# Kernel optimization log

Hardware: AMD Instinct MI355X
Metric: run time of the kernel (lower is better)

The kernel has to match this reference:

```python
import jax, jax.numpy as jnp
import numpy as np

# ---------- constants ----------
EPS = 1e-5
_rng = np.random.default_rng(0)
_P = _rng.normal(size=(8, 3))
_P /= np.linalg.norm(_P, axis=1, keepdims=True)

def _y2_np(p):
    x, y, z = p[:, 0], p[:, 1], p[:, 2]
    return np.stack([x * y, y * z, 3 * z * z - 1, x * z, x * x - y * y], axis=-1)

_A2 = np.linalg.pinv(_y2_np(_P)).astype(np.float32)  # [5,8]
P_C = jnp.asarray(_P.astype(np.float32))
A2_C = jnp.asarray(_A2)
NORM_CONST = np.float32(1.0 / np.sqrt(20.0))  # avg_num_neighbors ** -0.5
# res update (buffer zeros, not learnable): sigmoid(0)=0.5
_U = 0.5
C_OLD = np.float32(1.0 / np.sqrt(_U * _U + 1.0))
C_NEW = np.float32(_U * C_OLD)


def _y2(p):  # real l=2 monomial basis on unit vectors
    x, y, z = p[..., 0], p[..., 1], p[..., 2]
    return jnp.stack([x * y, y * z, 3.0 * z * z - 1.0, x * z, x * x - y * y], axis=-1)


def _frame(v):  # [E,3] -> R [E,3,3] with R @ v_hat = z
    n = v / jnp.linalg.norm(v, axis=-1, keepdims=True)
    z = jnp.array([0.0, 0.0, 1.0], v.dtype)
    xa = jnp.array([1.0, 0.0, 0.0], v.dtype)
    a = jnp.where(jnp.abs(n[:, 2:3]) < 0.99, z, xa)
    e1 = jnp.cross(a, n)
    e1 = e1 / jnp.linalg.norm(e1, axis=-1, keepdims=True)
    e2 = jnp.cross(n, e1)
    return jnp.stack([e1, e2, n], axis=1)


def _wigner_d2(R):  # [E,3,3] -> D2 [E,5,5] via sample-point fit
    pts = jnp.einsum('pj,eij->epi', P_C, R)  # R @ p_k, [E,8,3]
    M = _y2(pts)  # [E,8,5] = Y_P @ D^T
    Dt = jnp.einsum('ap,epb->eab', A2_C, M)  # [E,5,5]
    return jnp.swapaxes(Dt, 1, 2)


def _sln(x, w0, b0, w1, w2):  # separable equivariant layernorm, 32x0e+16x1e+8x2e
    s = x[:, :32]
    v1 = x[:, 32:80].reshape(-1, 16, 3)
    v2 = x[:, 80:120].reshape(-1, 8, 5)
    mu = jnp.mean(s, axis=-1, keepdims=True)
    var = jnp.mean((s - mu) ** 2, axis=-1, keepdims=True)
    s = (s - mu) * jax.lax.rsqrt(var + EPS) * w0 + b0
    var1 = jnp.mean(v1 ** 2, axis=(1, 2))  # degree-balanced component variance
    var2 = jnp.mean(v2 ** 2, axis=(1, 2))
    inv = jax.lax.rsqrt(0.5 * (var1 + var2) + EPS)[:, None, None]
    v1 = v1 * inv * w1[None, :, None]
    v2 = v2 * inv * w2[None, :, None]
    return jnp.concatenate([s, v1.reshape(-1, 48), v2.reshape(-1, 40)], axis=-1)


def _ir_linear(x, W0, b0, W1, W2):  # irreps-wise linear 32x0e+16x1e+8x2e -> same
    s = x[:, :32] @ (W0 / np.sqrt(32.0)) + b0
    v1 = jnp.einsum('eui,uv->evi', x[:, 32:80].reshape(-1, 16, 3), W1) / np.sqrt(16.0)
    v2 = jnp.einsum('eui,uv->evi', x[:, 80:120].reshape(-1, 8, 5), W2) / np.sqrt(8.0)
    return jnp.concatenate([s, v1.reshape(-1, 48), v2.reshape(-1, 40)], axis=-1)


def _so2(x_cat, R, D2f, D2b, w):  # SO2 linear with per-edge dynamic weights
    E = x_cat.shape[0]
    w0 = w[:, :8960].reshape(E, 112, 80)
    w1r = w[:, 8960:10112].reshape(E, 48, 24)
    w1i = w[:, 10112:11264].reshape(E, 48, 24)
    w2r = w[:, 11264:11392].reshape(E, 16, 8)
    w2i = w[:, 11392:11520].reshape(E, 16, 8)
    # split concatenated [in + hidden] blocks
    s = jnp.concatenate([x_cat[:, :32], x_cat[:, 120:152]], axis=-1)  # [E,64]
    v1 = jnp.concatenate([x_cat[:, 32:80].reshape(E, 16, 3),
                          x_cat[:, 152:200].reshape(E, 16, 3)], axis=1)  # [E,32,3]
    v2 = jnp.concatenate([x_cat[:, 80:120].reshape(E, 8, 5),
                          x_cat[:, 200:240].reshape(E, 16 // 2, 5)], axis=1)  # [E,16,5]
    # rotate into edge-aligned frame
    v1 = jnp.einsum('eij,euj->eui', R, v1)
    v2 = jnp.einsum('eij,euj->eui', D2f, v2)
    in0 = jnp.concatenate([s, v1[:, :, 1], v2[:, :, 2]], axis=-1)   # m=0, [E,112]
    inn1 = jnp.concatenate([v1[:, :, 0], v2[:, :, 1]], axis=-1)     # m=-1, [E,48]
    inp1 = jnp.concatenate([v1[:, :, 2], v2[:, :, 3]], axis=-1)     # m=+1
    inn2 = v2[:, :, 0]  # m=-2
    inp2 = v2[:, :, 4]  # m=+2
    out0 = jnp.einsum('ei,eio->eo', in0, w0) / np.sqrt(112.0)
    op1 = (jnp.einsum('ei,eio->eo', inp1, w1r) - jnp.einsum('ei,eio->eo', inn1, w1i)) / np.sqrt(48.0)
    on1 = (jnp.einsum('ei,eio->eo', inn1, w1r) + jnp.einsum('ei,eio->eo', inp1, w1i)) / np.sqrt(48.0)
    op2 = (jnp.einsum('ei,eio->eo', inp2, w2r) - jnp.einsum('ei,eio->eo', inn2, w2i)) / np.sqrt(16.0)
    on2 = (jnp.einsum('ei,eio->eo', inn2, w2r) + jnp.einsum('ei,eio->eo', inp2, w2i)) / np.sqrt(16.0)
    s_out = out0[:, :56]
    y1 = jnp.stack([on1[:, :16], out0[:, 56:72], op1[:, :16]], axis=-1)  # [E,16,3]
    y2o = jnp.stack([on2, on1[:, 16:24], out0[:, 72:80], op1[:, 16:24], op2], axis=-1)  # [E,8,5]
    # rotate back
    y1 = jnp.einsum('eij,euj->eui', jnp.swapaxes(R, 1, 2), y1)
    y2o = jnp.einsum('eij,euj->eui', D2b, y2o)
    return jnp.concatenate([s_out, y1.reshape(E, 48), y2o.reshape(E, 40)], axis=-1)  # [E,144]


def _gate(m):  # 32x0e scalars | 24x0e gates | 16x1e+8x2e gated
    s = jax.nn.silu(m[:, :32])
    g = jax.nn.sigmoid(m[:, 32:56])
    v1 = m[:, 56:104].reshape(-1, 16, 3) * g[:, :16, None]
    v2 = m[:, 104:144].reshape(-1, 8, 5) * g[:, 16:24, None]
    return jnp.concatenate([s, v1.reshape(-1, 48), v2.reshape(-1, 40)], axis=-1)


def _env(m, we):  # E3ElementLinear: per-mul elementwise weights
    s = m[:, :32] * we[:, :32]
    v1 = m[:, 32:80].reshape(-1, 16, 3) * we[:, 32:48, None]
    v2 = m[:, 80:120].reshape(-1, 8, 5) * we[:, 48:56, None]
    return jnp.concatenate([s, v1.reshape(-1, 48), v2.reshape(-1, 40)], axis=-1)


def setup_inputs() -> dict:
    key = jax.random.key(0)
    ks = jax.random.split(key, 16)
    N, E, L = 512, 10240, 128
    inp = {
        'latents': jax.random.normal(ks[0], (E, L), jnp.float32),
        'node_features': jax.random.normal(ks[1], (N, 120), jnp.float32),
        'hidden_features': jax.random.normal(ks[2], (E, 120), jnp.float32),
        'node_onehot': jnp.ones((N, 16), jnp.float32),
        'edge_vector': jax.random.normal(ks[3], (E, 3), jnp.float32),
        'W_tp': jax.random.normal(ks[4], (L, 11520), jnp.float32),
        'W_env': jax.random.normal(ks[5], (L, 56), jnp.float32),
        'sln_w0': jnp.ones((32,), jnp.float32),
        'sln_b0': jnp.zeros((32,), jnp.float32),
        'sln_w1': jnp.ones((16,), jnp.float32),
        'sln_w2': jnp.ones((8,), jnp.float32),
        'Wp0': jax.random.normal(ks[6], (32, 32), jnp.float32),
        'bp0': jnp.zeros((32,), jnp.float32),
        'Wp1': jax.random.normal(ks[7], (16, 16), jnp.float32),
        'Wp2': jax.random.normal(ks[8], (8, 8), jnp.float32),
        'Wr0': jax.random.normal(ks[9], (32, 32), jnp.float32),
        'br0': jnp.zeros((32,), jnp.float32),
        'Wr1': jax.random.normal(ks[10], (16, 16), jnp.float32),
        'Wr2': jax.random.normal(ks[11], (8, 8), jnp.float32),
        'atom_type': jax.random.randint(ks[12], (N,), 0, 10, jnp.int32),
        'edge_index': jax.random.randint(ks[13], (2, E), 0, N, jnp.int32),
        'active_edges': jnp.arange(E, dtype=jnp.int32),
    }
    return inp


def reference(latents, node_features, hidden_features, node_onehot, edge_vector,
              W_tp, W_env, sln_w0, sln_b0, sln_w1, sln_w2,
              Wp0, bp0, Wp1, Wp2, Wr0, br0, Wr1, Wr2,
              atom_type, edge_index, active_edges):
    n_nodes = node_features.shape[0]
    center = edge_index[0][active_edges]
    nf = _sln(node_features, sln_w0, sln_b0, sln_w1, sln_w2)
    x_cat = jnp.concatenate([nf[center], hidden_features], axis=-1)  # [E,240]
    v = edge_vector[active_edges]
    R = _frame(v)
    D2f = _wigner_d2(R)
    D2b = _wigner_d2(jnp.swapaxes(R, 1, 2))
    wdyn = latents @ (W_tp / np.sqrt(128.0))  # per-edge dynamic SO2 weights
    msg = _so2(x_cat, R, D2f, D2b, wdyn)
    msg = _gate(msg)
    msg = _ir_linear(msg, Wp0, bp0, Wp1, Wp2)
    wenv = latents[active_edges] @ (W_env / np.sqrt(128.0))
    weighted = _env(msg, wenv)
    new_nf = jax.ops.segment_sum(weighted, center, num_segments=n_nodes)
    new_nf = new_nf * NORM_CONST
    res = _ir_linear(node_features, Wr0, br0, Wr1, Wr2)
    return C_NEW * new_nf + C_OLD * res
```

## Files before the change

### kernel.cpp

```cpp
#include <hip/hip_runtime.h>
#include <math.h>

#define E_TOT   10240
#define N_NODES 512
#define NCOL    11520

typedef unsigned short ushort_t;
typedef unsigned int   uint_t;
typedef __bf16 bf16x8 __attribute__((ext_vector_type(8)));
typedef float  f32x4  __attribute__((ext_vector_type(4)));

constexpr float EPSF        = 1e-5f;
constexpr float INV_SQRT128 = 0.08838834764831845f;
constexpr float INV_SQRT112 = 0.09449111825230681f;
constexpr float INV_SQRT48  = 0.14433756729740643f;
constexpr float INV_SQRT32  = 0.17677669529663687f;
constexpr float INV_SQRT16  = 0.25f;
constexpr float INV_SQRT8   = 0.35355339059327373f;
constexpr float SC0 = INV_SQRT128 * INV_SQRT112;
constexpr float SC1 = INV_SQRT128 * INV_SQRT48;
constexpr float SC2 = INV_SQRT128 * INV_SQRT16;
constexpr float C_OLD_ = 0.8944271909999159f;
constexpr float C_NEW_ = 0.4472135954999579f;
constexpr float NORMC  = 0.22360679774997896f;

__device__ __forceinline__ float wsum(float v) {
#pragma unroll
  for (int off = 32; off > 0; off >>= 1) v += __shfl_xor(v, off, 64);
  return v;
}

__device__ __forceinline__ ushort_t f2bf(float x) {
  uint_t u = __float_as_uint(x);
  u = (u + 0x7fffu + ((u >> 16) & 1u)) >> 16;
  return (ushort_t)u;
}

__device__ __forceinline__ void wigner5(const float q[9], float D[25]) {
  const float q0x=q[0],q0y=q[1],q0z=q[2];
  const float q1x=q[3],q1y=q[4],q1z=q[5];
  const float q2x=q[6],q2y=q[7],q2z=q[8];
  D[0]  = q0x*q1y + q1x*q0y;
  D[1]  = q0y*q1z + q1y*q0z;
  D[2]  = 0.5f*(q0z*q1z);
  D[3]  = q0x*q1z + q1x*q0z;
  D[4]  = 0.5f*(q0x*q1x - q0y*q1y);
  D[5]  = q1x*q2y + q2x*q1y;
  D[6]  = q1y*q2z + q2y*q1z;
  D[7]  = 0.5f*(q1z*q2z);
  D[8]  = q1x*q2z + q2x*q1z;
  D[9]  = 0.5f*(q1x*q2x - q1y*q2y);
  D[10] = 6.f*q2x*q2y;
  D[11] = 6.f*q2y*q2z;
  D[12] = 0.5f*(3.f*q2z*q2z - 1.f);
  D[13] = 6.f*q2x*q2z;
  D[14] = 1.5f*(q2x*q2x - q2y*q2y);
  D[15] = q0x*q2y + q2x*q0y;
  D[16] = q0y*q2z + q2y*q0z;
  D[17] = 0.5f*(q0z*q2z);
  D[18] = q0x*q2z + q2x*q0z;
  D[19] = 0.5f*(q0x*q2x - q0y*q2y);
  D[20] = 2.f*(q0x*q0y - q1x*q1y);
  D[21] = 2.f*(q0y*q0z - q1y*q1z);
  D[22] = 0.5f*(q0z*q0z - q1z*q1z);
  D[23] = 2.f*(q0x*q0z - q1x*q1z);
  D[24] = 0.5f*((q0x*q0x - q1x*q1x) - (q0y*q0y - q1y*q1y));
}

__global__ void k0_latpack(const float* __restrict__ lat,
                           ushort_t* __restrict__ lath, ushort_t* __restrict__ latl) {
  int idx = blockIdx.x*256 + threadIdx.x;
  if (idx >= E_TOT*128) return;
  float x = lat[idx];
  ushort_t h = f2bf(x);
  float hf = __uint_as_float(((uint_t)h) << 16);
  lath[idx] = h;
  latl[idx] = f2bf(x - hf);
}

__global__ void k_pack(const float* __restrict__ Wtp, ushort_t* __restrict__ Wp) {
  const int nt = blockIdx.x;
  const int t = threadIdx.x;
  const int kc = t >> 6, lane = t & 63;
  const int m = lane & 15, kg = lane >> 4;
  int col, tt;
  if (nt < 560)      { col = nt/112; tt = nt - col*112; }
  else if (nt < 608) { col = 5;  tt = nt-560; }
  else if (nt < 632) { col = 6;  tt = nt-608; }
  else if (nt < 680) { col = 7;  tt = nt-632; }
  else if (nt < 704) { col = 8;  tt = nt-680; }
  else if (nt < 712) { col = 9;  tt = nt-704; }
  else               { col = 10; tt = nt-712; }
  int c; float sc;
  switch (col) {
    case 5:  c = 8960  + tt*24 + m;                      sc = SC1; break;
    case 6:  c = 8960  + (2*tt + (m>>3))*24 + 16 + (m&7); sc = SC1; break;
    case 7:  c = 10112 + tt*24 + m;                      sc = SC1; break;
    case 8:  c = 10112 + (2*tt + (m>>3))*24 + 16 + (m&7); sc = SC1; break;
    case 9:  c = 11264 + (2*tt + (m>>3))*8 + (m&7);      sc = SC2; break;
    case 10: c = 11392 + (2*tt + (m>>3))*8 + (m&7);      sc = SC2; break;
    default: c = tt*80 + col*16 + m;                     sc = SC0; break;
  }
  ushort_t hi[8], lo[8];
#pragma unroll
  for (int jj = 0; jj < 8; ++jj) {
    int l = kc*32 + kg*8 + jj;
    float w = Wtp[(size_t)l*NCOL + c] * sc;
    ushort_t h = f2bf(w);
    float hf = __uint_as_float(((uint_t)h) << 16);
    hi[jj] = h;
    lo[jj] = f2bf(w - hf);
  }
  size_t base = ((size_t)nt*8 + kc*2)*512 + (size_t)lane*8;
#pragma unroll
  for (int jj = 0; jj < 8; ++jj) {
    Wp[base + jj]       = hi[jj];
    Wp[base + 512 + jj] = lo[jj];
  }
}

__global__ void k1_sln(const float* __restrict__ x_all,
                       const float* __restrict__ w0, const float* __restrict__ b0,
                       const float* __restrict__ w1, const float* __restrict__ w2,
                       float* __restrict__ nf) {
  const int n = blockIdx.x;
  const int t = threadIdx.x;
  const float* x = x_all + n*120;
  float xs = (t < 32) ? x[t] : 0.f;
  float ssum = wsum(xs);
  float ssq  = wsum(xs*xs);
  float mu   = ssum * (1.f/32.f);
  float var  = ssq * (1.f/32.f) - mu*mu;
  float istd = rsqrtf(var + EPSF);
  float q1 = (t < 48) ? x[32+t] : 0.f;
  float v1s = wsum(q1*q1);
  float q2 = (t < 40) ? x[80+t] : 0.f;
  float v2s = wsum(q2*q2);
  float inv = rsqrtf(0.5f*(v1s*(1.f/48.f) + v2s*(1.f/40.f)) + EPSF);
  for (int j = t; j < 120; j += 64) {
    float val = x[j], r;
    if (j < 32)      r = (val - mu)*istd*w0[j] + b0[j];
    else if (j < 80) r = val*inv*w1[(j-32)/3];
    else             r = val*inv*w2[(j-80)/5];
    nf[n*120 + j] = r;
  }
}

__global__ void k2_edge_prep(const float* __restrict__ hid,
                             const float* __restrict__ evec,
                             const int*   __restrict__ eidx,
                             const int*   __restrict__ act,
                             const float* __restrict__ nf,
                             float* __restrict__ invT,
                             float* __restrict__ Rm,
                             float* __restrict__ D2bm) {
  const int e = blockIdx.x*blockDim.x + threadIdx.x;
  if (e >= E_TOT) return;
  const int ae  = act[e];
  const int ctr = eidx[ae];
  float vx = evec[ae*3+0], vy = evec[ae*3+1], vz = evec[ae*3+2];
  float rn = rsqrtf(vx*vx + vy*vy + vz*vz);
  float nx = vx*rn, ny = vy*rn, nz = vz*rn;
  float e1x, e1y, e1z;
  if (fabsf(nz) < 0.99f) { e1x = -ny; e1y = nx;  e1z = 0.f; }
  else                   { e1x = 0.f; e1y = -nz; e1z = ny;  }
  float rl = rsqrtf(e1x*e1x + e1y*e1y + e1z*e1z);
  e1x *= rl; e1y *= rl; e1z *= rl;
  float e2x = ny*e1z - nz*e1y;
  float e2y = nz*e1x - nx*e1z;
  float e2z = nx*e1y - ny*e1x;
  float R[9] = {e1x,e1y,e1z, e2x,e2y,e2z, nx,ny,nz};
#pragma unroll
  for (int j = 0; j < 9; ++j) Rm[e*9 + j] = R[j];
  float Df[25];
  wigner5(R, Df);
  float Rt[9] = {R[0],R[3],R[6], R[1],R[4],R[7], R[2],R[5],R[8]};
  float Db[25];
  wigner5(Rt, Db);
#pragma unroll
  for (int j = 0; j < 25; ++j) D2bm[e*25 + j] = Db[j];
  const float* xa = nf  + (size_t)ctr*120;
  const float* xb = hid + (size_t)e*120;
#define IVST(r_, v_) invT[(size_t)(r_)*E_TOT + e] = (v_)
#pragma unroll
  for (int j = 0; j < 32; ++j) { IVST(j, xa[j]); IVST(32+j, xb[j]); }
#pragma unroll
  for (int u = 0; u < 32; ++u) {
    const float* src = (u < 16) ? (xa + 32 + 3*u) : (xb + 32 + 3*(u-16));
    float px = src[0], py = src[1], pz = src[2];
    float rx = R[0]*px + R[1]*py + R[2]*pz;
    float ry = R[3]*px + R[4]*py + R[5]*pz;
    float rz = R[6]*px + R[7]*py + R[8]*pz;
    IVST(64+u, ry);
    IVST(112+u, rx);
    IVST(160+u, rz);
  }
#pragma unroll
  for (int u = 0; u < 16; ++u) {
    const float* src = (u < 8) ? (xa + 80 + 5*u) : (xb + 80 + 5*(u-8));
    float p0 = src[0], p1 = src[1], p2 = src[2], p3 = src[3], p4 = src[4];
    float d[5];
#pragma unroll
    for (int i = 0; i < 5; ++i)
      d[i] = Df[i*5+0]*p0 + Df[i*5+1]*p1 + Df[i*5+2]*p2 + Df[i*5+3]*p3 + Df[i*5+4]*p4;
    IVST(96+u,  d[2]);
    IVST(144+u, d[1]);
    IVST(192+u, d[3]);
    IVST(208+u, d[0]);
    IVST(224+u, d[4]);
  }
#undef IVST
}

__global__ void k2_wenv(const float* __restrict__ lat, const float* __restrict__ Wenv,
                        const int* __restrict__ act, float* __restrict__ wenvo) {
  const int e = blockIdx.x*4 + (threadIdx.x >> 6);
  const int o = threadIdx.x & 63;
  if (o >= 56) return;
  const int ae = act[e];
  const float* lrow = lat + (size_t)ae*128;
  float s = 0.f;
  for (int l = 0; l < 128; ++l) s += lrow[l]*Wenv[l*56 + o];
  wenvo[(size_t)e*56 + o] = s * INV_SQRT128;
}

template<bool TWO, bool PAIR>
__device__ __forceinline__ void run_seg(
    const bf16x8* __restrict__ W8, int f0, int f1, int tstart,
    int multP, int multN, int slotP, int slotN, float sgnP,
    const float* __restrict__ in_lds,
    const bf16x8 (&Bh)[4][2], const bf16x8 (&Bl)[4][2],
    int lane, int e0, float* __restrict__ oa) {
  const int le = lane & 15, g = lane >> 4, gh = g >> 1;
  f32x4 aP0 = {0,0,0,0}, aP1 = {0,0,0,0}, aN0 = {0,0,0,0}, aN1 = {0,0,0,0};
  for (int f = f0; f < f1; ++f) {
    const bf16x8* ap = W8 + (size_t)f*512 + lane;
    f32x4 d0 = {0,0,0,0}, d1 = {0,0,0,0};
#pragma unroll
    for (int kc = 0; kc < 4; ++kc) {
      bf16x8 Ah = ap[(kc*2+0)*64];
      bf16x8 Al = ap[(kc*2+1)*64];
      d0 = __builtin_amdgcn_mfma_f32_16x16x32_bf16(Ah, Bh[kc][0], d0, 0, 0, 0);
      d1 = __builtin_amdgcn_mfma_f32_16x16x32_bf16(Ah, Bh[kc][1], d1, 0, 0, 0);
      d0 = __builtin_amdgcn_mfma_f32_16x16x32_bf16(Ah, Bl[kc][0], d0, 0, 0, 0);
      d1 = __builtin_amdgcn_mfma_f32_16x16x32_bf16(Ah, Bl[kc][1], d1, 0, 0, 0);
      d0 = __builtin_amdgcn_mfma_f32_16x16x32_bf16(Al, Bh[kc][0], d0, 0, 0, 0);
      d1 = __builtin_amdgcn_mfma_f32_16x16x32_bf16(Al, Bh[kc][1], d1, 0, 0, 0);
    }
    int tt = f - tstart;
    int idx = PAIR ? (2*tt + gh) : tt;
    float mP0 = in_lds[(multP+idx)*32 + le];
    float mP1 = in_lds[(multP+idx)*32 + 16 + le];
#pragma unroll
    for (int r = 0; r < 4; ++r) { aP0[r] += mP0*d0[r]; aP1[r] += mP1*d1[r]; }
    if (TWO) {
      float mN0 = in_lds[(multN+idx)*32 + le];
      float mN1 = in_lds[(multN+idx)*32 + 16 + le];
#pragma unroll
      for (int r = 0; r < 4; ++r) { aN0[r] += mN0*d0[r]; aN1[r] += mN1*d1[r]; }
    }
  }
#pragma unroll
  for (int r = 0; r < 4; ++r) {
    int mm = g*4 + r;
    int sp = slotP + (PAIR ? (mm & 7) : mm);
    atomicAdd(&oa[(size_t)e0*144 + sp], sgnP*aP0[r]);
    atomicAdd(&oa[(size_t)(e0+16)*144 + sp], sgnP*aP1[r]);
    if (TWO) {
      int sn = slotN + (PAIR ? (mm & 7) : mm);
      atomicAdd(&oa[(size_t)e0*144 + sn], aN0[r]);
      atomicAdd(&oa[(size_t)(e0+16)*144 + sn], aN1[r]);
    }
  }
}

__global__ __launch_bounds__(256, 4)
void k3_gemm(const ushort_t* __restrict__ Wp,
             const ushort_t* __restrict__ lath,
             const ushort_t* __restrict__ latl,
             const float*  __restrict__ invT,
             float* __restrict__ oa_g) {
  __shared__ float in_lds[240*32];
  const int t = threadIdx.x;
  const int eb = blockIdx.x;
  for (int i = t; i < 240*32; i += 256) {
    int r = i >> 5, e = i & 31;
    in_lds[i] = invT[(size_t)r*E_TOT + eb*32 + e];
  }
  const int wave = t >> 6, lane = t & 63;
  const int le = lane & 15, g = lane >> 4;
  bf16x8 Bh[4][2], Bl[4][2];
  {
    const int e0 = eb*32 + le;
    const int ko = g*8;
#pragma unroll
    for (int kc = 0; kc < 4; ++kc) {
#pragma unroll
      for (int n = 0; n < 2; ++n) {
        size_t off = (size_t)(e0 + 16*n)*128 + kc*32 + ko;
        Bh[kc][n] = *(const bf16x8*)(lath + off);
        Bl[kc][n] = *(const bf16x8*)(latl + off);
      }
    }
  }
  __syncthreads();
  const bf16x8* W8 = (const bf16x8*)Wp;
  const int e0 = eb*32 + le;
  const int f0 = (blockIdx.y*4 + wave)*45, f1 = f0 + 45;
  int lo, hi;
#pragma unroll
  for (int col = 0; col < 5; ++col) {
    int s = col*112, epos = s + 112;
    lo = f0 > s ? f0 : s; hi = f1 < epos ? f1 : epos;
    if (lo < hi)
      run_seg<false,false>(W8, lo, hi, s, 0, 0, col*16, 0, 1.f,
                           in_lds, Bh, Bl, lane, e0, oa_g);
  }
  lo = f0 > 560 ? f0 : 560; hi = f1 < 608 ? f1 : 608;
  if (lo < hi) run_seg<true,false>(W8, lo, hi, 560, 160, 112, 80, 104, 1.f,
                                   in_lds, Bh, Bl, lane, e0, oa_g);
  lo = f0 > 608 ? f0 : 608; hi = f1 < 632 ? f1 : 632;
  if (lo < hi) run_seg<true,true>(W8, lo, hi, 608, 160, 112, 96, 120, 1.f,
                                  in_lds, Bh, Bl, lane, e0, oa_g);
  lo = f0 > 632 ? f0 : 632; hi = f1 < 680 ? f1 : 680;
  if (lo < hi) run_seg<true,false>(W8, lo, hi, 632, 112, 160, 80, 104, -1.f,
                                   in_lds, Bh, Bl, lane, e0, oa_g);
  lo = f0 > 680 ? f0 : 680; hi = f1 < 704 ? f1 : 704;
  if (lo < hi) run_seg<true,true>(W8, lo, hi, 680, 112, 160, 96, 120, -1.f,
                                  in_lds, Bh, Bl, lane, e0, oa_g);
  lo = f0 > 704 ? f0 : 704; hi = f1 < 712 ? f1 : 712;
  if (lo < hi) run_seg<true,true>(W8, lo, hi, 704, 224, 208, 128, 136, 1.f,
                                  in_lds, Bh, Bl, lane, e0, oa_g);
  lo = f0 > 712 ? f0 : 712; hi = f1 < 720 ? f1 : 720;
  if (lo < hi) run_seg<true,true>(W8, lo, hi, 712, 208, 224, 128, 136, -1.f,
                                  in_lds, Bh, Bl, lane, e0, oa_g);
}

__global__ __launch_bounds__(256)
void k4_epi(const float* __restrict__ oa_g, const float* __restrict__ Rm,
            const float* __restrict__ D2bm, const float* __restrict__ wenvg,
            const int* __restrict__ eidx, const int* __restrict__ act,
            const float* __restrict__ Wp0, const float* __restrict__ bp0,
            const float* __restrict__ Wp1, const float* __restrict__ Wp2,
            float* __restrict__ accg) {
  __shared__ float sc[4][160];
  const int wave = threadIdx.x >> 6, lane = threadIdx.x & 63;
  const int eg = blockIdx.x*4 + wave;
  const float* o_ = oa_g + (size_t)eg*144;
  if (lane < 56) {
    float v = o_[lane];
    sc[wave][lane] = (lane < 32) ? v/(1.f + expf(-v)) : 1.f/(1.f + expf(-v));
  }
  __syncthreads();
  const float* Rr = Rm + (size_t)eg*9;
  const float* Db = D2bm + (size_t)eg*25;
  if (lane < 48) {
    int u = lane/3, cc = lane - u*3;
    float yx = o_[104+u], yy = o_[56+u], yz = o_[80+u];
    float p = Rr[cc]*yx + Rr[3+cc]*yy + Rr[6+cc]*yz;
    sc[wave][56+lane] = p * sc[wave][32+u];
  }
  __syncthreads();
  if (lane < 40) {
    int u = lane/5, ii = lane - u*5;
    float y0 = o_[136+u], y1v = o_[120+u], y2v = o_[72+u], y3 = o_[96+u], y4 = o_[128+u];
    float p = Db[ii*5+0]*y0 + Db[ii*5+1]*y1v + Db[ii*5+2]*y2v + Db[ii*5+3]*y3 + Db[ii*5+4]*y4;
    sc[wave][104+lane] = p * sc[wave][48+u];
  }
  __syncthreads();
  const float* we = wenvg + (size_t)eg*56;
  const int ctr = eidx[act[eg]];
  float* dst = accg + (size_t)ctr*120;
#pragma unroll
  for (int rnd = 0; rnd < 2; ++rnd) {
    int jo = rnd*64 + lane;
    if (jo < 120) {
      float val;
      if (jo < 32) {
        float s = 0.f;
#pragma unroll
        for (int i2 = 0; i2 < 32; ++i2) s += sc[wave][i2]*Wp0[i2*32 + jo];
        val = (s*INV_SQRT32 + bp0[jo]) * we[jo];
      } else if (jo < 80) {
        int jj = jo-32, v = jj/3, cc = jj - v*3;
        float s = 0.f;
#pragma unroll
        for (int u = 0; u < 16; ++u) s += sc[wave][56 + u*3 + cc]*Wp1[u*16 + v];
        val = s*INV_SQRT16*we[32+v];
      } else {
        int jj = jo-80, v = jj/5, ii = jj - v*5;
        float s = 0.f;
#pragma unroll
        for (int u = 0; u < 8; ++u) s += sc[wave][104 + u*5 + ii]*Wp2[u*8 + v];
        val = s*INV_SQRT8*we[48+v];
      }
      atomicAdd(&dst[jo], val);
    }
  }
}

__global__ void k5_final(const float* __restrict__ x_all,
                         const float* __restrict__ Wr0, const float* __restrict__ br0,
                         const float* __restrict__ Wr1, const float* __restrict__ Wr2,
                         const float* __restrict__ accg,
                         float* __restrict__ out) {
  const int n = blockIdx.x;
  const int t = threadIdx.x;
  if (t >= 120) return;
  const float* x = x_all + n*120;
  float r;
  if (t < 32) {
    float s = 0.f;
#pragma unroll
    for (int i = 0; i < 32; ++i) s += x[i]*Wr0[i*32 + t];
    r = s*INV_SQRT32 + br0[t];
  } else if (t < 80) {
    int j = t - 32, v = j/3, cp = j - 3*v;
    float s = 0.f;
#pragma unroll
    for (int u = 0; u < 16; ++u) s += x[32 + u*3 + cp]*Wr1[u*16 + v];
    r = s*INV_SQRT16;
  } else {
    int j = t - 80, v = j/5, cp = j - 5*v;
    float s = 0.f;
#pragma unroll
    for (int u = 0; u < 8; ++u) s += x[80 + u*5 + cp]*Wr2[u*8 + v];
    r = s*INV_SQRT8;
  }
  out[n*120 + t] = C_NEW_*(NORMC*accg[n*120 + t]) + C_OLD_*r;
}

extern "C" void kernel_launch(void* const* d_in, const int* in_sizes, int n_in,
                              void* d_out, int out_size, void* d_ws, size_t ws_size,
                              hipStream_t stream) {
  const float* lat  = (const float*)d_in[0];
  const float* ndf  = (const float*)d_in[1];
  const float* hid  = (const float*)d_in[2];
  const float* evec = (const float*)d_in[4];
  const float* Wtp  = (const float*)d_in[5];
  const float* Wenv = (const float*)d_in[6];
  const float* w0   = (const float*)d_in[7];
  const float* b0   = (const float*)d_in[8];
  const float* w1   = (const float*)d_in[9];
  const float* w2   = (const float*)d_in[10];
  const float* Wp0  = (const float*)d_in[11];
  const float* bp0  = (const float*)d_in[12];
  const float* Wp1  = (const float*)d_in[13];
  const float* Wp2  = (const float*)d_in[14];
  const float* Wr0  = (const float*)d_in[15];
  const float* br0  = (const float*)d_in[16];
  const float* Wr1  = (const float*)d_in[17];
  const float* Wr2  = (const float*)d_in[18];
  const int*   eidx = (const int*)d_in[20];
  const int*   act  = (const int*)d_in[21];
  float* out = (float*)d_out;

  char* p = (char*)d_ws;
  float*    nf    = (float*)(p);
  float*    invT  = (float*)(p + 245760);
  float*    Rm    = (float*)(p + 10076160);
  float*    D2bm  = (float*)(p + 10444800);
  float*    wenv  = (float*)(p + 11468800);
  float*    accg  = (float*)(p + 13762560);
  float*    oa_g  = (float*)(p + 14008320);
  ushort_t* lath  = (ushort_t*)(p + 19906560);
  ushort_t* latl  = (ushort_t*)(p + 22528000);
  ushort_t* Wpack = (ushort_t*)(p + 25149440);

  hipMemsetAsync(accg, 0, 245760, stream);
  hipMemsetAsync(oa_g, 0, 5898240, stream);
  k0_latpack<<<(E_TOT*128 + 255)/256, 256, 0, stream>>>(lat, lath, latl);
  k_pack<<<720, 256, 0, stream>>>(Wtp, Wpack);
  k1_sln<<<N_NODES, 64, 0, stream>>>(ndf, w0, b0, w1, w2, nf);
  k2_edge_prep<<<E_TOT/256, 256, 0, stream>>>(hid, evec, eidx, act, nf, invT, Rm, D2bm);
  k2_wenv<<<E_TOT/4, 256, 0, stream>>>(lat, Wenv, act, wenv);
  k3_gemm<<<dim3(E_TOT/32, 4), 256, 0, stream>>>(Wpack, lath, latl, invT, oa_g);
  k4_epi<<<E_TOT/4, 256, 0, stream>>>(oa_g, Rm, D2bm, wenv, eidx, act, Wp0, bp0, Wp1, Wp2, accg);
  k5_final<<<N_NODES, 128, 0, stream>>>(ndf, Wr0, br0, Wr1, Wr2, accg, out);
}
```

Baseline: 344.1 us.

## Share weight tiles across waves via double-buffered LDS and retile wenv GEMM

The SO2 GEMM kernel now gives each block 128 edges (32 per wave) and a range of 80 weight tiles. Weight tiles are staged once per block into a double-buffered LDS ring with register prefetch, so the four waves share them instead of each streaming its own from global memory. The per-edge input multipliers are read straight from global memory rather than staged in LDS, and occupancy is lowered to 2 blocks per CU. The wenv kernel is rewritten so each thread computes one edge's 56 outputs from LDS-cached weights, which removes the repeated global reads of Wenv but adds a 56-float accumulator per thread (register pressure).

Measured after the change: 301.3 us. 1.14x faster.

```diff
diff --git a/kernel.cpp b/kernel.cpp
--- a/kernel.cpp
+++ b/kernel.cpp
@@ -93,13 +93,13 @@
   else               { col = 10; tt = nt-712; }
   int c; float sc;
   switch (col) {
-    case 5:  c = 8960  + tt*24 + m;                      sc = SC1; break;
+    case 5:  c = 8960  + tt*24 + m;                       sc = SC1; break;
     case 6:  c = 8960  + (2*tt + (m>>3))*24 + 16 + (m&7); sc = SC1; break;
-    case 7:  c = 10112 + tt*24 + m;                      sc = SC1; break;
+    case 7:  c = 10112 + tt*24 + m;                       sc = SC1; break;
     case 8:  c = 10112 + (2*tt + (m>>3))*24 + 16 + (m&7); sc = SC1; break;
-    case 9:  c = 11264 + (2*tt + (m>>3))*8 + (m&7);      sc = SC2; break;
-    case 10: c = 11392 + (2*tt + (m>>3))*8 + (m&7);      sc = SC2; break;
-    default: c = tt*80 + col*16 + m;                     sc = SC0; break;
+    case 9:  c = 11264 + (2*tt + (m>>3))*8 + (m&7);       sc = SC2; break;
+    case 10: c = 11392 + (2*tt + (m>>3))*8 + (m&7);       sc = SC2; break;
+    default: c = tt*80 + col*16 + m;                      sc = SC0; break;
   }
   ushort_t hi[8], lo[8];
 #pragma unroll
@@ -212,128 +212,152 @@
 #undef IVST
 }
 
-__global__ void k2_wenv(const float* __restrict__ lat, const float* __restrict__ Wenv,
-                        const int* __restrict__ act, float* __restrict__ wenvo) {
-  const int e = blockIdx.x*4 + (threadIdx.x >> 6);
-  const int o = threadIdx.x & 63;
-  if (o >= 56) return;
-  const int ae = act[e];
-  const float* lrow = lat + (size_t)ae*128;
-  float s = 0.f;
-  for (int l = 0; l < 128; ++l) s += lrow[l]*Wenv[l*56 + o];
-  wenvo[(size_t)e*56 + o] = s * INV_SQRT128;
-}
-
-template<bool TWO, bool PAIR>
-__device__ __forceinline__ void run_seg(
-    const bf16x8* __restrict__ W8, int f0, int f1, int tstart,
-    int multP, int multN, int slotP, int slotN, float sgnP,
-    const float* __restrict__ in_lds,
-    const bf16x8 (&Bh)[4][2], const bf16x8 (&Bl)[4][2],
-    int lane, int e0, float* __restrict__ oa) {
-  const int le = lane & 15, g = lane >> 4, gh = g >> 1;
-  f32x4 aP0 = {0,0,0,0}, aP1 = {0,0,0,0}, aN0 = {0,0,0,0}, aN1 = {0,0,0,0};
-  for (int f = f0; f < f1; ++f) {
-    const bf16x8* ap = W8 + (size_t)f*512 + lane;
-    f32x4 d0 = {0,0,0,0}, d1 = {0,0,0,0};
-#pragma unroll
-    for (int kc = 0; kc < 4; ++kc) {
-      bf16x8 Ah = ap[(kc*2+0)*64];
-      bf16x8 Al = ap[(kc*2+1)*64];
-      d0 = __builtin_amdgcn_mfma_f32_16x16x32_bf16(Ah, Bh[kc][0], d0, 0, 0, 0);
-      d1 = __builtin_amdgcn_mfma_f32_16x16x32_bf16(Ah, Bh[kc][1], d1, 0, 0, 0);
-      d0 = __builtin_amdgcn_mfma_f32_16x16x32_bf16(Ah, Bl[kc][0], d0, 0, 0, 0);
-      d1 = __builtin_amdgcn_mfma_f32_16x16x32_bf16(Ah, Bl[kc][1], d1, 0, 0, 0);
-      d0 = __builtin_amdgcn_mfma_f32_16x16x32_bf16(Al, Bh[kc][0], d0, 0, 0, 0);
-      d1 = __builtin_amdgcn_mfma_f32_16x16x32_bf16(Al, Bh[kc][1], d1, 0, 0, 0);
-    }
-    int tt = f - tstart;
-    int idx = PAIR ? (2*tt + gh) : tt;
-    float mP0 = in_lds[(multP+idx)*32 + le];
-    float mP1 = in_lds[(multP+idx)*32 + 16 + le];
-#pragma unroll
-    for (int r = 0; r < 4; ++r) { aP0[r] += mP0*d0[r]; aP1[r] += mP1*d1[r]; }
-    if (TWO) {
-      float mN0 = in_lds[(multN+idx)*32 + le];
-      float mN1 = in_lds[(multN+idx)*32 + 16 + le];
-#pragma unroll
-      for (int r = 0; r < 4; ++r) { aN0[r] += mN0*d0[r]; aN1[r] += mN1*d1[r]; }
-    }
-  }
-#pragma unroll
-  for (int r = 0; r < 4; ++r) {
-    int mm = g*4 + r;
-    int sp = slotP + (PAIR ? (mm & 7) : mm);
-    atomicAdd(&oa[(size_t)e0*144 + sp], sgnP*aP0[r]);
-    atomicAdd(&oa[(size_t)(e0+16)*144 + sp], sgnP*aP1[r]);
-    if (TWO) {
-      int sn = slotN + (PAIR ? (mm & 7) : mm);
-      atomicAdd(&oa[(size_t)e0*144 + sn], aN0[r]);
-      atomicAdd(&oa[(size_t)(e0+16)*144 + sn], aN1[r]);
-    }
-  }
-}
-
-__global__ __launch_bounds__(256, 4)
+__global__ __launch_bounds__(256)
+void k2_wenv(const float* __restrict__ lat, const float* __restrict__ Wenv,
+             const int* __restrict__ act, float* __restrict__ wenvo) {
+  __shared__ float Wl[128*56];
+  __shared__ float latc[256*17];
+  __shared__ int   aes[256];
+  const int t = threadIdx.x;
+  const int e0 = blockIdx.x*256;
+  for (int i = t; i < 128*56; i += 256) Wl[i] = Wenv[i];
+  aes[t] = act[e0 + t];
+  float acc[56];
+#pragma unroll
+  for (int o = 0; o < 56; ++o) acc[o] = 0.f;
+  for (int lc = 0; lc < 8; ++lc) {
+    __syncthreads();
+    for (int i = t; i < 256*16; i += 256) {
+      int el = i >> 4, j = i & 15;
+      latc[el*17 + j] = lat[(size_t)aes[el]*128 + lc*16 + j];
+    }
+    __syncthreads();
+#pragma unroll
+    for (int j = 0; j < 16; ++j) {
+      float lv = latc[t*17 + j];
+      const float* wr = &Wl[(lc*16 + j)*56];
+#pragma unroll
+      for (int o = 0; o < 56; ++o) acc[o] += lv * wr[o];
+    }
+  }
+  float* dst = wenvo + (size_t)(e0 + t)*56;
+#pragma unroll
+  for (int o = 0; o < 56; ++o) dst[o] = acc[o] * INV_SQRT128;
+}
+
+__global__ __launch_bounds__(256, 2)
 void k3_gemm(const ushort_t* __restrict__ Wp,
              const ushort_t* __restrict__ lath,
              const ushort_t* __restrict__ latl,
              const float*  __restrict__ invT,
              float* __restrict__ oa_g) {
-  __shared__ float in_lds[240*32];
+  __shared__ __align__(16) ushort_t abuf[2][8192];
   const int t = threadIdx.x;
-  const int eb = blockIdx.x;
-  for (int i = t; i < 240*32; i += 256) {
-    int r = i >> 5, e = i & 31;
-    in_lds[i] = invT[(size_t)r*E_TOT + eb*32 + e];
-  }
   const int wave = t >> 6, lane = t & 63;
-  const int le = lane & 15, g = lane >> 4;
+  const int le = lane & 15, g = lane >> 4, gh = g >> 1;
+  const int fbase = blockIdx.y * 80;
+  const int e0w = blockIdx.x*128 + wave*32;
   bf16x8 Bh[4][2], Bl[4][2];
-  {
-    const int e0 = eb*32 + le;
-    const int ko = g*8;
-#pragma unroll
-    for (int kc = 0; kc < 4; ++kc) {
-#pragma unroll
-      for (int n = 0; n < 2; ++n) {
-        size_t off = (size_t)(e0 + 16*n)*128 + kc*32 + ko;
-        Bh[kc][n] = *(const bf16x8*)(lath + off);
-        Bl[kc][n] = *(const bf16x8*)(latl + off);
+#pragma unroll
+  for (int kc = 0; kc < 4; ++kc)
+#pragma unroll
+    for (int n = 0; n < 2; ++n) {
+      size_t off = (size_t)(e0w + n*16 + le)*128 + kc*32 + g*8;
+      Bh[kc][n] = *(const bf16x8*)(lath + off);
+      Bl[kc][n] = *(const bf16x8*)(latl + off);
+    }
+  int col, tt;
+  if (fbase < 560)      { col = fbase/112; tt = fbase - col*112; }
+  else if (fbase < 608) { col = 5;  tt = fbase-560; }
+  else if (fbase < 632) { col = 6;  tt = fbase-608; }
+  else if (fbase < 680) { col = 7;  tt = fbase-632; }
+  else if (fbase < 704) { col = 8;  tt = fbase-680; }
+  else if (fbase < 712) { col = 9;  tt = fbase-704; }
+  else                  { col = 10; tt = fbase-712; }
+  int mP_, mN_, sP_, sN_, segLen; float sg_; bool PAIR_, TWO_;
+  auto setParams = [&](int cf) {
+    if (cf < 5)       { segLen=112; mP_=0;   mN_=0;   sP_=cf*16; sN_=0;   sg_=1.f;  PAIR_=false; TWO_=false; }
+    else if (cf == 5) { segLen=48;  mP_=160; mN_=112; sP_=80;  sN_=104; sg_=1.f;  PAIR_=false; TWO_=true; }
+    else if (cf == 6) { segLen=24;  mP_=160; mN_=112; sP_=96;  sN_=120; sg_=1.f;  PAIR_=true;  TWO_=true; }
+    else if (cf == 7) { segLen=48;  mP_=112; mN_=160; sP_=80;  sN_=104; sg_=-1.f; PAIR_=false; TWO_=true; }
+    else if (cf == 8) { segLen=24;  mP_=112; mN_=160; sP_=96;  sN_=120; sg_=-1.f; PAIR_=true;  TWO_=true; }
+    else if (cf == 9) { segLen=8;   mP_=224; mN_=208; sP_=128; sN_=136; sg_=1.f;  PAIR_=true;  TWO_=true; }
+    else              { segLen=8;   mP_=208; mN_=224; sP_=128; sN_=136; sg_=-1.f; PAIR_=true;  TWO_=true; }
+  };
+  setParams(col);
+  f32x4 aP0={0,0,0,0}, aP1={0,0,0,0}, aN0={0,0,0,0}, aN1={0,0,0,0};
+  auto flush = [&]() {
+#pragma unroll
+    for (int r = 0; r < 4; ++r) {
+      int mm = g*4 + r;
+      int sp = sP_ + (PAIR_ ? (mm & 7) : mm);
+      atomicAdd(&oa_g[(size_t)(e0w + le)*144 + sp], sg_*aP0[r]);
+      atomicAdd(&oa_g[(size_t)(e0w + 16 + le)*144 + sp], sg_*aP1[r]);
+      if (TWO_) {
+        int sn = sN_ + (PAIR_ ? (mm & 7) : mm);
+        atomicAdd(&oa_g[(size_t)(e0w + le)*144 + sn], aN0[r]);
+        atomicAdd(&oa_g[(size_t)(e0w + 16 + le)*144 + sn], aN1[r]);
       }
     }
+    aP0 = (f32x4){0,0,0,0}; aP1 = (f32x4){0,0,0,0};
+    aN0 = (f32x4){0,0,0,0}; aN1 = (f32x4){0,0,0,0};
+  };
+#pragma unroll
+  for (int qq = 0; qq < 4; ++qq) {
+    uint4 v = *(const uint4*)(Wp + ((size_t)fbase*8 + wave*4 + qq)*512 + lane*8);
+    *(uint4*)&abuf[0][(wave*4 + qq)*512 + lane*8] = v;
   }
   __syncthreads();
-  const bf16x8* W8 = (const bf16x8*)Wp;
-  const int e0 = eb*32 + le;
-  const int f0 = (blockIdx.y*4 + wave)*45, f1 = f0 + 45;
-  int lo, hi;
-#pragma unroll
-  for (int col = 0; col < 5; ++col) {
-    int s = col*112, epos = s + 112;
-    lo = f0 > s ? f0 : s; hi = f1 < epos ? f1 : epos;
-    if (lo < hi)
-      run_seg<false,false>(W8, lo, hi, s, 0, 0, col*16, 0, 1.f,
-                           in_lds, Bh, Bl, lane, e0, oa_g);
-  }
-  lo = f0 > 560 ? f0 : 560; hi = f1 < 608 ? f1 : 608;
-  if (lo < hi) run_seg<true,false>(W8, lo, hi, 560, 160, 112, 80, 104, 1.f,
-                                   in_lds, Bh, Bl, lane, e0, oa_g);
-  lo = f0 > 608 ? f0 : 608; hi = f1 < 632 ? f1 : 632;
-  if (lo < hi) run_seg<true,true>(W8, lo, hi, 608, 160, 112, 96, 120, 1.f,
-                                  in_lds, Bh, Bl, lane, e0, oa_g);
-  lo = f0 > 632 ? f0 : 632; hi = f1 < 680 ? f1 : 680;
-  if (lo < hi) run_seg<true,false>(W8, lo, hi, 632, 112, 160, 80, 104, -1.f,
-                                   in_lds, Bh, Bl, lane, e0, oa_g);
-  lo = f0 > 680 ? f0 : 680; hi = f1 < 704 ? f1 : 704;
-  if (lo < hi) run_seg<true,true>(W8, lo, hi, 680, 112, 160, 96, 120, -1.f,
-                                  in_lds, Bh, Bl, lane, e0, oa_g);
-  lo = f0 > 704 ? f0 : 704; hi = f1 < 712 ? f1 : 712;
-  if (lo < hi) run_seg<true,true>(W8, lo, hi, 704, 224, 208, 128, 136, 1.f,
-                                  in_lds, Bh, Bl, lane, e0, oa_g);
-  lo = f0 > 712 ? f0 : 712; hi = f1 < 720 ? f1 : 720;
-  if (lo < hi) run_seg<true,true>(W8, lo, hi, 712, 208, 224, 128, 136, -1.f,
-                                  in_lds, Bh, Bl, lane, e0, oa_g);
+  for (int c = 0; c < 40; ++c) {
+    const int cb = c & 1, nb = cb ^ 1;
+    uint4 pre[4];
+    const bool more = (c + 1) < 40;
+    if (more) {
+#pragma unroll
+      for (int qq = 0; qq < 4; ++qq)
+        pre[qq] = *(const uint4*)(Wp + ((size_t)(fbase + 2*(c+1))*8 + wave*4 + qq)*512 + lane*8);
+    }
+#pragma unroll
+    for (int lt = 0; lt < 2; ++lt) {
+      int idx = PAIR_ ? (2*tt + gh) : tt;
+      int rowP = mP_ + idx;
+      float mP0 = invT[(size_t)rowP*E_TOT + e0w + le];
+      float mP1 = invT[(size_t)rowP*E_TOT + e0w + 16 + le];
+      float mN0 = 0.f, mN1 = 0.f;
+      if (TWO_) {
+        int rowN = mN_ + idx;
+        mN0 = invT[(size_t)rowN*E_TOT + e0w + le];
+        mN1 = invT[(size_t)rowN*E_TOT + e0w + 16 + le];
+      }
+      f32x4 d0 = {0,0,0,0}, d1 = {0,0,0,0};
+#pragma unroll
+      for (int kc = 0; kc < 4; ++kc) {
+        bf16x8 Ah = *(const bf16x8*)&abuf[cb][(lt*8 + kc*2 + 0)*512 + lane*8];
+        bf16x8 Al = *(const bf16x8*)&abuf[cb][(lt*8 + kc*2 + 1)*512 + lane*8];
+        d0 = __builtin_amdgcn_mfma_f32_16x16x32_bf16(Ah, Bh[kc][0], d0, 0, 0, 0);
+        d1 = __builtin_amdgcn_mfma_f32_16x16x32_bf16(Ah, Bh[kc][1], d1, 0, 0, 0);
+        d0 = __builtin_amdgcn_mfma_f32_16x16x32_bf16(Ah, Bl[kc][0], d0, 0, 0, 0);
+        d1 = __builtin_amdgcn_mfma_f32_16x16x32_bf16(Ah, Bl[kc][1], d1, 0, 0, 0);
+        d0 = __builtin_amdgcn_mfma_f32_16x16x32_bf16(Al, Bh[kc][0], d0, 0, 0, 0);
+        d1 = __builtin_amdgcn_mfma_f32_16x16x32_bf16(Al, Bh[kc][1], d1, 0, 0, 0);
+      }
+#pragma unroll
+      for (int r = 0; r < 4; ++r) { aP0[r] += mP0*d0[r]; aP1[r] += mP1*d1[r]; }
+      if (TWO_) {
+#pragma unroll
+        for (int r = 0; r < 4; ++r) { aN0[r] += mN0*d0[r]; aN1[r] += mN1*d1[r]; }
+      }
+      tt++;
+      if (tt == segLen) { flush(); col++; tt = 0; setParams(col); }
+    }
+    if (more) {
+#pragma unroll
+      for (int qq = 0; qq < 4; ++qq)
+        *(uint4*)&abuf[nb][(wave*4 + qq)*512 + lane*8] = pre[qq];
+    }
+    __syncthreads();
+  }
+  if (tt > 0) flush();
 }
 
 __global__ __launch_bounds__(256)
@@ -473,8 +497,8 @@
   k_pack<<<720, 256, 0, stream>>>(Wtp, Wpack);
   k1_sln<<<N_NODES, 64, 0, stream>>>(ndf, w0, b0, w1, w2, nf);
   k2_edge_prep<<<E_TOT/256, 256, 0, stream>>>(hid, evec, eidx, act, nf, invT, Rm, D2bm);
-  k2_wenv<<<E_TOT/4, 256, 0, stream>>>(lat, Wenv, act, wenv);
-  k3_gemm<<<dim3(E_TOT/32, 4), 256, 0, stream>>>(Wpack, lath, latl, invT, oa_g);
+  k2_wenv<<<E_TOT/256, 256, 0, stream>>>(lat, Wenv, act, wenv);
+  k3_gemm<<<dim3(E_TOT/128, 9), 256, 0, stream>>>(Wpack, lath, latl, invT, oa_g);
   k4_epi<<<E_TOT/4, 256, 0, stream>>>(oa_g, Rm, D2bm, wenv, eidx, act, Wp0, bp0, Wp1, Wp2, accg);
   k5_final<<<N_NODES, 128, 0, stream>>>(ndf, Wr0, br0, Wr1, Wr2, accg, out);
 }
```
